# Optimization experiments

Hardware: AMD Instinct MI355X
Metric: run time of the kernel (lower is better)

Reference implementation:

```python
import jax, jax.numpy as jnp
import numpy as np

B, S_ENC, S_DEC = 4, 2048, 1024
ENC_DIM, DEC_DIM, H = 1024, 1024, 16
CROSS_DIM = max(ENC_DIM, DEC_DIM)
HEAD_DIM_DEC = DEC_DIM // H
SCALE = HEAD_DIM_DEC ** 0.5  # module divides by dec_scaling only


def _linear_params(key, d_in, d_out):
    kw, kb = jax.random.split(key)
    bound = 1.0 / np.sqrt(d_in)
    W = jax.random.uniform(kw, (d_in, d_out), jnp.float32, -bound, bound)
    b = jax.random.uniform(kb, (d_out,), jnp.float32, -bound, bound)
    return W, b


def setup_inputs() -> dict:
    key = jax.random.key(0)
    ks = jax.random.split(key, 7)
    enc = jax.random.normal(ks[0], (B, S_ENC, ENC_DIM), jnp.float32)
    dec = jax.random.normal(ks[1], (B, S_DEC, DEC_DIM), jnp.float32)
    enc_mask = jax.random.uniform(ks[2], (B, 1, 1, S_ENC)) < 0.1
    q_w, q_b = _linear_params(ks[3], DEC_DIM, CROSS_DIM)
    k_w, k_b = _linear_params(ks[4], ENC_DIM, CROSS_DIM)
    v_w, v_b = _linear_params(ks[5], ENC_DIM, DEC_DIM)
    o_w, o_b = _linear_params(ks[6], DEC_DIM, DEC_DIM)
    return {"enc": enc, "enc_mask": enc_mask, "dec": dec,
            "q_w": q_w, "q_b": q_b, "k_w": k_w, "k_b": k_b,
            "v_w": v_w, "v_b": v_b, "o_w": o_w, "o_b": o_b}


def _split_heads(x):
    b, s, d = x.shape
    return x.reshape(b, s, H, d // H).transpose(0, 2, 1, 3)  # [b,h,s,hd]


def reference(enc, enc_mask, dec, q_w, q_b, k_w, k_b, v_w, v_b, o_w, o_b):
    q = _split_heads(dec @ q_w + q_b)   # [B,H,Sq,cross_hd]
    k = _split_heads(enc @ k_w + k_b)   # [B,H,Sk,cross_hd]
    v = _split_heads(enc @ v_w + v_b)   # [B,H,Sk,dec_hd]
    logits = jnp.einsum('bhqd,bhkd->bhqk', q, k) / SCALE
    logits = jnp.where(enc_mask, -jnp.inf, logits)
    a = jax.nn.softmax(logits, axis=-1)
    x = jnp.einsum('bhqk,bhkd->bhqd', a, v)          # [B,H,Sq,dec_hd]
    x = x.transpose(0, 2, 1, 3).reshape(x.shape[0], x.shape[2], -1)  # [B,Sq,DEC_DIM]
    return x @ o_w + o_b
```

## Files before the change

kernel.cpp:

```cpp
#include <hip/hip_runtime.h>
#include <hip/hip_bf16.h>
#include <cstdint>

#define BB   4
#define SENC 2048
#define SDEC 1024
#define DM   1024
#define NH   16
#define HD   64

using short8 = __attribute__((ext_vector_type(8))) short;
using f32x4  = __attribute__((ext_vector_type(4))) float;

__device__ inline unsigned short f2bf(float f) {
    return (unsigned short)((__builtin_bit_cast(unsigned int, f) + 0x8000u) >> 16);
}
__device__ inline unsigned int pk2bf(float a, float b) {
    return ((__builtin_bit_cast(unsigned int, a) + 0x8000u) >> 16) |
           ((__builtin_bit_cast(unsigned int, b) + 0x8000u) & 0xffff0000u);
}

__device__ inline float fexp2(float x) {
#if __has_builtin(__builtin_amdgcn_exp2f)
    return __builtin_amdgcn_exp2f(x);
#else
    return exp2f(x);
#endif
}

#if __has_builtin(__builtin_amdgcn_global_load_lds)
#define HAS_GLL 1
#endif

__device__ inline void stage16(const void* g, void* l) {
#ifdef HAS_GLL
    typedef __attribute__((address_space(1))) const unsigned int guint;
    typedef __attribute__((address_space(3))) unsigned int luint;
    __builtin_amdgcn_global_load_lds((guint*)g, (luint*)l, 16, 0, 0);
#else
    *(short8*)l = *(const short8*)g;
#endif
}

__global__ __launch_bounds__(256) void prep_kernel(
    const float* __restrict__ dec, const float* __restrict__ enc,
    unsigned short* __restrict__ actb,
    const float* __restrict__ qw, const float* __restrict__ kw,
    const float* __restrict__ vw, const float* __restrict__ ow,
    unsigned short* __restrict__ qwt, unsigned short* __restrict__ kvwt,
    unsigned short* __restrict__ owt) {
    __shared__ float t[64][65];
    const int id = blockIdx.x, tid = threadIdx.x;
    if (id < 12288) {
        const int nd = BB * SDEC * DM;
        int i = (id * 256 + tid) * 4;
        const float* src = (i < nd) ? (dec + i) : (enc + (i - nd));
        float4 v = *(const float4*)src;
        ushort4 o;
        o.x = f2bf(v.x); o.y = f2bf(v.y); o.z = f2bf(v.z); o.w = f2bf(v.w);
        *(ushort4*)(actb + i) = o;
        return;
    }
    const int id2 = id - 12288;
    const int z = id2 >> 8, ky = (id2 >> 4) & 15, nx = id2 & 15;
    const float* src; unsigned short* dst;
    switch (z) {
        case 0:  src = qw; dst = qwt; break;
        case 1:  src = kw; dst = kvwt; break;
        case 2:  src = vw; dst = kvwt + (size_t)64 * 16384; break;
        default: src = ow; dst = owt; break;
    }
    const int k0 = ky * 64, n0 = nx * 64;
    #pragma unroll
    for (int it = 0; it < 16; ++it) {
        int e = it * 256 + tid, r = e >> 6, c = e & 63;
        t[r][c] = src[(size_t)(k0 + r) * DM + n0 + c];
    }
    __syncthreads();
    #pragma unroll
    for (int it = 0; it < 16; ++it) {
        int e = it * 256 + tid, r = e >> 6, c = e & 63;
        size_t off = (size_t)((n0 + r) >> 4) * 16384 + (size_t)((k0 + c) >> 3) * 128
                   + ((r & 15) << 3) + (c & 7);
        dst[off] = f2bf(t[c][r]);
    }
}

__global__ __launch_bounds__(256) void gemm_qkv_kernel(
    const unsigned short* __restrict__ encb, const unsigned short* __restrict__ decb,
    const unsigned short* __restrict__ kvwt, const unsigned short* __restrict__ qwt,
    const float* __restrict__ q_b, const float* __restrict__ k_b, const float* __restrict__ v_b,
    unsigned short* __restrict__ Qb, unsigned short* __restrict__ Kb,
    unsigned short* __restrict__ Vtb) {
    __shared__ __align__(16) unsigned short As[2][128 * 32];
    const int id = blockIdx.x;
    const bool isKV = id < 1024;
    const unsigned short *A, *Bw;
    int m0, n0;
    if (isKV) {
        const int x = id & 7, w = id >> 3;
        A = encb; Bw = kvwt;
        m0 = (x * 8 + (w >> 4)) * 128;
        n0 = (w & 15) * 128;
    } else {
        const int i2 = id - 1024, x = i2 & 7, w = i2 >> 3;
        A = decb; Bw = qwt;
        m0 = (x * 4 + (w >> 3)) * 128;
        n0 = (w & 7) * 128;
    }
    const int tid = threadIdx.x;
    const int wave = tid >> 6, lane = tid & 63, quad = lane >> 4, l16 = lane & 15;
    const int wr = wave >> 1, wc = wave & 1;
    const int r16 = lane >> 2, c8 = (lane & 3) * 8;
    f32x4 acc[4][4] = {};

    const unsigned short* Bbase = Bw + (size_t)(n0 >> 4) * 16384 + (size_t)(wc * 4) * 16384
                                + quad * 128 + l16 * 8;
    short8 bcur[4], bnxt[4];
    #pragma unroll
    for (int j = 0; j < 4; ++j) bcur[j] = *(const short8*)&Bbase[j * 16384];

    #pragma unroll
    for (int i = 0; i < 2; ++i) {
        const int row = wave * 32 + i * 16 + r16;
        stage16(&A[(size_t)(m0 + row) * DM + c8], &As[0][row * 32 + c8]);
    }
    for (int it = 0; it < 32; ++it) {
        const int bf = it & 1;
        __syncthreads();
        if (it < 31) {
            const int kb2 = (it + 1) * 32, nb = bf ^ 1;
            #pragma unroll
            for (int i = 0; i < 2; ++i) {
                const int row = wave * 32 + i * 16 + r16;
                stage16(&A[(size_t)(m0 + row) * DM + kb2 + c8], &As[nb][row * 32 + c8]);
            }
            #pragma unroll
            for (int j = 0; j < 4; ++j)
                bnxt[j] = *(const short8*)&Bbase[j * 16384 + kb2 * 16];
        }
        short8 af[4];
        #pragma unroll
        for (int i = 0; i < 4; ++i) af[i] = *(const short8*)&As[bf][(wr * 64 + i * 16 + l16) * 32 + quad * 8];
        #pragma unroll
        for (int i = 0; i < 4; ++i)
            #pragma unroll
            for (int j = 0; j < 4; ++j)
                acc[i][j] = __builtin_amdgcn_mfma_f32_16x16x32_bf16(af[i], bcur[j], acc[i][j], 0, 0, 0);
        #pragma unroll
        for (int j = 0; j < 4; ++j) bcur[j] = bnxt[j];
    }
    #pragma unroll
    for (int i = 0; i < 4; ++i) {
        #pragma unroll
        for (int j = 0; j < 4; ++j) {
            const int gc = n0 + wc * 64 + j * 16 + l16;
            const int gr0 = m0 + wr * 64 + i * 16 + quad * 4;
            if (!isKV) {
                const float bv = q_b[gc];
                const int h = gc >> 6, d = gc & 63;
                #pragma unroll
                for (int rr = 0; rr < 4; ++rr) {
                    int gr = gr0 + rr, b = gr >> 10, sq = gr & 1023;
                    float v = (acc[i][j][rr] + bv) * 0.18033688011112042f;
                    Qb[(((size_t)(b * NH + h) * SDEC + sq) << 6) + d] = f2bf(v);
                }
            } else if (gc < 1024) {
                const float bv = k_b[gc];
                const int h = gc >> 6, d = gc & 63;
                #pragma unroll
                for (int rr = 0; rr < 4; ++rr) {
                    int gr = gr0 + rr, b = gr >> 11, sk = gr & 2047;
                    size_t off = (size_t)(b * NH + h) * 131072 + (size_t)(sk >> 4) * 1024
                               + ((d >> 3) << 7) + ((sk & 15) << 3) + (d & 7);
                    Kb[off] = f2bf(acc[i][j][rr] + bv);
                }
            } else {
                const int gc2 = gc & 1023;
                const float bv = v_b[gc2];
                const int h = gc2 >> 6, d = gc2 & 63;
                const int b = gr0 >> 11, sk0 = gr0 & 2047;
                size_t off = (size_t)(b * NH + h) * 131072 + (size_t)(d >> 4) * 32768
                           + (size_t)(sk0 >> 3) * 128 + ((d & 15) << 3) + (sk0 & 7);
                uint2 pk;
                pk.x = pk2bf(acc[i][j][0] + bv, acc[i][j][1] + bv);
                pk.y = pk2bf(acc[i][j][2] + bv, acc[i][j][3] + bv);
                *(uint2*)&Vtb[off] = pk;
            }
        }
    }
}

__global__ __launch_bounds__(256) void gemm_o_kernel(const unsigned short* __restrict__ A,
                                                     const unsigned short* __restrict__ Bw,
                                                     const float* __restrict__ bias,
                                                     float* __restrict__ Cout) {
    __shared__ __align__(16) unsigned short As[2][64 * 32];
    const int id = blockIdx.x, x = id & 7, w = id >> 3;
    const int m0 = (x * 8 + (w >> 3)) * 64, n0 = (w & 7) * 128;
    const int tid = threadIdx.x;
    const int wave = tid >> 6, lane = tid & 63, quad = lane >> 4, l16 = lane & 15;
    const int r16 = lane >> 2, c8 = (lane & 3) * 8;
    f32x4 acc[4][2] = {};
    const unsigned short* Bbase = Bw + (size_t)((n0 >> 4) + wave * 2) * 16384 + quad * 128 + l16 * 8;
    short8 bcur[2], bnxt[2];
    #pragma unroll
    for (int j = 0; j < 2; ++j) bcur[j] = *(const short8*)&Bbase[j * 16384];
    {
        const int rowA = wave * 16 + r16;
        stage16(&A[(size_t)(m0 + rowA) * DM + c8], &As[0][rowA * 32 + c8]);
    }
    for (int it = 0; it < 32; ++it) {
        const int bf = it & 1;
        __syncthreads();
        if (it < 31) {
            const int kb2 = (it + 1) * 32, nb = bf ^ 1;
            const int rowA = wave * 16 + r16;
            stage16(&A[(size_t)(m0 + rowA) * DM + kb2 + c8], &As[nb][rowA * 32 + c8]);
            #pragma unroll
            for (int j = 0; j < 2; ++j) bnxt[j] = *(const short8*)&Bbase[j * 16384 + kb2 * 16];
        }
        short8 af[4];
        #pragma unroll
        for (int i = 0; i < 4; ++i) af[i] = *(const short8*)&As[bf][(i * 16 + l16) * 32 + quad * 8];
        #pragma unroll
        for (int i = 0; i < 4; ++i)
            #pragma unroll
            for (int j = 0; j < 2; ++j)
                acc[i][j] = __builtin_amdgcn_mfma_f32_16x16x32_bf16(af[i], bcur[j], acc[i][j], 0, 0, 0);
        #pragma unroll
        for (int j = 0; j < 2; ++j) bcur[j] = bnxt[j];
    }
    #pragma unroll
    for (int i = 0; i < 4; ++i)
        #pragma unroll
        for (int j = 0; j < 2; ++j) {
            const int gc = n0 + wave * 32 + j * 16 + l16;
            const float bv = bias[gc];
            #pragma unroll
            for (int rr = 0; rr < 4; ++rr) {
                const int gr = m0 + i * 16 + quad * 4 + rr;
                Cout[(size_t)gr * DM + gc] = acc[i][j][rr] + bv;
            }
        }
}

__global__ __launch_bounds__(256) void attn_kernel(const unsigned short* __restrict__ Qb,
                                                   const unsigned short* __restrict__ Kb,
                                                   const unsigned short* __restrict__ Vtb,
                                                   const int* __restrict__ mask,
                                                   unsigned short* __restrict__ Xb) {
    __shared__ __align__(16) unsigned short Ps[4][16 * 72];
    const int id = blockIdx.x, x = id & 7, r = id >> 3;
    const int bh = x * 8 + (r & 7), qt = r >> 3;
    const int b = bh >> 4, h = bh & 15;
    const int q0 = qt * 128;
    const int tid = threadIdx.x, wave = tid >> 6, lane = tid & 63;
    const int quad = lane >> 4, l16 = lane & 15;
    const int lo = quad * 128 + l16 * 8;

    const unsigned short* Kfp = Kb + (size_t)bh * 131072;
    const unsigned short* Vfp = Vtb + (size_t)bh * 131072;
    const int* mp = mask + (size_t)b * SENC;

    short8 qf[2][2];
    {
        const unsigned short* Qp = Qb + ((size_t)bh * SDEC + q0 + wave * 32) * HD;
        #pragma unroll
        for (int g = 0; g < 2; ++g) {
            qf[g][0] = *(const short8*)&Qp[(g * 16 + l16) * HD + quad * 8];
            qf[g][1] = *(const short8*)&Qp[(g * 16 + l16) * HD + 32 + quad * 8];
        }
    }

    float lsum[2] = {0.f, 0.f};
    f32x4 o[2][4] = {};

    for (int kb = 0; kb < SENC; kb += 64) {
        short8 kA0[4], kA1[4], vB0[4], vB1[4];
        const unsigned short* kt = Kfp + (size_t)(kb >> 4) * 1024 + lo;
        const unsigned short* vt = Vfp + (size_t)(kb >> 3) * 128 + lo;
        #pragma unroll
        for (int j = 0; j < 4; ++j) {
            kA0[j] = *(const short8*)&kt[j * 1024];
            kA1[j] = *(const short8*)&kt[j * 1024 + 512];
            vB0[j] = *(const short8*)&vt[j * 32768];
            vB1[j] = *(const short8*)&vt[j * 32768 + 512];
        }
        int4 mi[4];
        #pragma unroll
        for (int j = 0; j < 4; ++j) mi[j] = *(const int4*)&mp[kb + j * 16 + quad * 4];
        #pragma unroll
        for (int g = 0; g < 2; ++g) {
            f32x4 st[4];
            #pragma unroll
            for (int j = 0; j < 4; ++j) {
                f32x4 z = {0.f, 0.f, 0.f, 0.f};
                z = __builtin_amdgcn_mfma_f32_16x16x32_bf16(kA0[j], qf[g][0], z, 0, 0, 0);
                st[j] = __builtin_amdgcn_mfma_f32_16x16x32_bf16(kA1[j], qf[g][1], z, 0, 0, 0);
            }
            #pragma unroll
            for (int j = 0; j < 4; ++j) {
                float p0 = mi[j].x ? 0.f : fexp2(st[j][0]);
                float p1 = mi[j].y ? 0.f : fexp2(st[j][1]);
                float p2 = mi[j].z ? 0.f : fexp2(st[j][2]);
                float p3 = mi[j].w ? 0.f : fexp2(st[j][3]);
                lsum[g] += (p0 + p1) + (p2 + p3);
                uint2 pkv;
                pkv.x = pk2bf(p0, p1);
                pkv.y = pk2bf(p2, p3);
                *(uint2*)&Ps[wave][l16 * 72 + j * 16 + quad * 4] = pkv;
            }
            asm volatile("s_waitcnt lgkmcnt(0)" ::: "memory");
            short8 pA0 = *(const short8*)&Ps[wave][l16 * 72 + quad * 8];
            short8 pA1 = *(const short8*)&Ps[wave][l16 * 72 + 32 + quad * 8];
            #pragma unroll
            for (int dj = 0; dj < 4; ++dj) {
                o[g][dj] = __builtin_amdgcn_mfma_f32_16x16x32_bf16(pA0, vB0[dj], o[g][dj], 0, 0, 0);
                o[g][dj] = __builtin_amdgcn_mfma_f32_16x16x32_bf16(pA1, vB1[dj], o[g][dj], 0, 0, 0);
            }
        }
    }
    #pragma unroll
    for (int g = 0; g < 2; ++g) {
        float lg = lsum[g];
        lg += __shfl_xor(lg, 16);
        lg += __shfl_xor(lg, 32);
        #pragma unroll
        for (int rr = 0; rr < 4; ++rr) {
            float iv = 1.0f / __shfl(lg, quad * 4 + rr, 64);
            int sq = q0 + wave * 32 + g * 16 + quad * 4 + rr;
            #pragma unroll
            for (int dj = 0; dj < 4; ++dj)
                Xb[((size_t)(b * SDEC) + sq) * DM + h * HD + dj * 16 + l16] = f2bf(o[g][dj][rr] * iv);
        }
    }
}

extern "C" void kernel_launch(void* const* d_in, const int* in_sizes, int n_in,
                              void* d_out, int out_size, void* d_ws, size_t ws_size,
                              hipStream_t stream) {
    const float* enc   = (const float*)d_in[0];
    const int*   emask = (const int*)d_in[1];
    const float* dec   = (const float*)d_in[2];
    const float* q_w   = (const float*)d_in[3];
    const float* q_b   = (const float*)d_in[4];
    const float* k_w   = (const float*)d_in[5];
    const float* k_b   = (const float*)d_in[6];
    const float* v_w   = (const float*)d_in[7];
    const float* v_b   = (const float*)d_in[8];
    const float* o_w   = (const float*)d_in[9];
    const float* o_b   = (const float*)d_in[10];
    float* out = (float*)d_out;

    char* ws = (char*)d_ws;
    unsigned short* decb = (unsigned short*)ws; ws += (size_t)4096 * 1024 * 2;
    unsigned short* encb = (unsigned short*)ws; ws += (size_t)8192 * 1024 * 2;
    unsigned short* qwt  = (unsigned short*)ws; ws += (size_t)1024 * 1024 * 2;
    unsigned short* kvwt = (unsigned short*)ws; ws += (size_t)2048 * 1024 * 2;
    unsigned short* owt  = (unsigned short*)ws; ws += (size_t)1024 * 1024 * 2;
    unsigned short* Qb   = (unsigned short*)ws; ws += (size_t)BB * NH * SDEC * HD * 2;
    unsigned short* Kb   = (unsigned short*)ws; ws += (size_t)BB * NH * SENC * HD * 2;
    unsigned short* Vtb  = (unsigned short*)ws; ws += (size_t)BB * NH * HD * SENC * 2;
    unsigned short* Xb   = (unsigned short*)ws; ws += (size_t)4096 * 1024 * 2;

    prep_kernel<<<13312, 256, 0, stream>>>(dec, enc, decb, q_w, k_w, v_w, o_w, qwt, kvwt, owt);
    gemm_qkv_kernel<<<1280, 256, 0, stream>>>(encb, decb, kvwt, qwt, q_b, k_b, v_b, Qb, Kb, Vtb);
    attn_kernel<<<512, 256, 0, stream>>>(Qb, Kb, Vtb, emask, Xb);
    gemm_o_kernel<<<512, 256, 0, stream>>>(Xb, owt, o_b, out);
}
```

Measured before the change: 253.9 us.

## Pre-swizzle activations into MFMA fragment layout and drop LDS staging in GEMMs

The prep kernel now writes dec/enc bf16 activations in the 16x8 fragment-tiled layout, and attention writes X in the same layout. Both GEMMs can then load A fragments directly from global memory into registers with register double-buffering, removing LDS staging and the per-iteration block barriers. Attention halves the query tile per block, which doubles the grid, and software-prefetches K. The mask is converted to an additive float bias, so the per-element select becomes an add before exp2. The costs are a transpose-like write pattern in prep and more global and L2 traffic, because A fragments are no longer shared through LDS across waves.

```diff
diff --git a/kernel.cpp b/kernel.cpp
--- a/kernel.cpp
+++ b/kernel.cpp
@@ -28,40 +28,50 @@
 #endif
 }
 
-#if __has_builtin(__builtin_amdgcn_global_load_lds)
-#define HAS_GLL 1
-#endif
-
-__device__ inline void stage16(const void* g, void* l) {
-#ifdef HAS_GLL
-    typedef __attribute__((address_space(1))) const unsigned int guint;
-    typedef __attribute__((address_space(3))) unsigned int luint;
-    __builtin_amdgcn_global_load_lds((guint*)g, (luint*)l, 16, 0, 0);
-#else
-    *(short8*)l = *(const short8*)g;
-#endif
+__device__ inline size_t frag_off(int m, int k) {
+    return (size_t)(m >> 4) * 16384 + (size_t)(k >> 3) * 128 + ((m & 15) << 3) + (k & 7);
 }
 
 __global__ __launch_bounds__(256) void prep_kernel(
     const float* __restrict__ dec, const float* __restrict__ enc,
-    unsigned short* __restrict__ actb,
+    unsigned short* __restrict__ decb, unsigned short* __restrict__ encb,
     const float* __restrict__ qw, const float* __restrict__ kw,
     const float* __restrict__ vw, const float* __restrict__ ow,
     unsigned short* __restrict__ qwt, unsigned short* __restrict__ kvwt,
-    unsigned short* __restrict__ owt) {
+    unsigned short* __restrict__ owt,
+    const int* __restrict__ mask, float* __restrict__ maskf) {
+    const int id = blockIdx.x, tid = threadIdx.x;
+    if (id < 3072) {
+        __shared__ unsigned short t[64][72];
+        const int rt = id >> 4, ct = id & 15, k0 = ct * 64;
+        const float* src; unsigned short* dst; int m0;
+        if (rt < 64) { src = dec; dst = decb; m0 = rt * 64; }
+        else         { src = enc; dst = encb; m0 = (rt - 64) * 64; }
+        #pragma unroll
+        for (int i = 0; i < 4; ++i) {
+            const int row = i * 16 + (tid >> 4), col4 = (tid & 15) * 4;
+            float4 v = *(const float4*)&src[(size_t)(m0 + row) * DM + k0 + col4];
+            ushort4 o;
+            o.x = f2bf(v.x); o.y = f2bf(v.y); o.z = f2bf(v.z); o.w = f2bf(v.w);
+            *(ushort4*)&t[row][col4] = o;
+        }
+        __syncthreads();
+        const int f = tid >> 3, sub = tid & 7;
+        const int mt = f >> 3, kc = f & 7;
+        const int row0 = mt * 16 + sub * 2;
+        short8 a = *(const short8*)&t[row0][kc * 8];
+        short8 b = *(const short8*)&t[row0 + 1][kc * 8];
+        size_t off = (size_t)(m0 / 16 + mt) * 16384 + (size_t)(k0 / 8 + kc) * 128 + sub * 16;
+        *(short8*)&dst[off] = a;
+        *(short8*)&dst[off + 8] = b;
+        return;
+    }
+    if (id == 4096) {
+        for (int j = tid; j < BB * SENC; j += 256) maskf[j] = mask[j] ? -1e30f : 0.0f;
+        return;
+    }
     __shared__ float t[64][65];
-    const int id = blockIdx.x, tid = threadIdx.x;
-    if (id < 12288) {
-        const int nd = BB * SDEC * DM;
-        int i = (id * 256 + tid) * 4;
-        const float* src = (i < nd) ? (dec + i) : (enc + (i - nd));
-        float4 v = *(const float4*)src;
-        ushort4 o;
-        o.x = f2bf(v.x); o.y = f2bf(v.y); o.z = f2bf(v.z); o.w = f2bf(v.w);
-        *(ushort4*)(actb + i) = o;
-        return;
-    }
-    const int id2 = id - 12288;
+    const int id2 = id - 3072;
     const int z = id2 >> 8, ky = (id2 >> 4) & 15, nx = id2 & 15;
     const float* src; unsigned short* dst;
     switch (z) {
@@ -92,7 +102,6 @@
     const float* __restrict__ q_b, const float* __restrict__ k_b, const float* __restrict__ v_b,
     unsigned short* __restrict__ Qb, unsigned short* __restrict__ Kb,
     unsigned short* __restrict__ Vtb) {
-    __shared__ __align__(16) unsigned short As[2][128 * 32];
     const int id = blockIdx.x;
     const bool isKV = id < 1024;
     const unsigned short *A, *Bw;
@@ -111,44 +120,33 @@
     const int tid = threadIdx.x;
     const int wave = tid >> 6, lane = tid & 63, quad = lane >> 4, l16 = lane & 15;
     const int wr = wave >> 1, wc = wave & 1;
-    const int r16 = lane >> 2, c8 = (lane & 3) * 8;
+    const int lo = quad * 128 + l16 * 8;
+    const unsigned short* Ap = A + (size_t)(m0 / 16 + wr * 4) * 16384 + lo;
+    const unsigned short* Bp = Bw + (size_t)(n0 / 16 + wc * 4) * 16384 + lo;
     f32x4 acc[4][4] = {};
-
-    const unsigned short* Bbase = Bw + (size_t)(n0 >> 4) * 16384 + (size_t)(wc * 4) * 16384
-                                + quad * 128 + l16 * 8;
-    short8 bcur[4], bnxt[4];
-    #pragma unroll
-    for (int j = 0; j < 4; ++j) bcur[j] = *(const short8*)&Bbase[j * 16384];
-
-    #pragma unroll
-    for (int i = 0; i < 2; ++i) {
-        const int row = wave * 32 + i * 16 + r16;
-        stage16(&A[(size_t)(m0 + row) * DM + c8], &As[0][row * 32 + c8]);
-    }
+    short8 ac[4], bc[4], an[4], bn[4];
+    #pragma unroll
+    for (int i = 0; i < 4; ++i) {
+        ac[i] = *(const short8*)&Ap[i * 16384];
+        bc[i] = *(const short8*)&Bp[i * 16384];
+    }
+    #pragma unroll 2
     for (int it = 0; it < 32; ++it) {
-        const int bf = it & 1;
-        __syncthreads();
         if (it < 31) {
-            const int kb2 = (it + 1) * 32, nb = bf ^ 1;
-            #pragma unroll
-            for (int i = 0; i < 2; ++i) {
-                const int row = wave * 32 + i * 16 + r16;
-                stage16(&A[(size_t)(m0 + row) * DM + kb2 + c8], &As[nb][row * 32 + c8]);
+            const int ko = (it + 1) * 512;
+            #pragma unroll
+            for (int i = 0; i < 4; ++i) {
+                an[i] = *(const short8*)&Ap[i * 16384 + ko];
+                bn[i] = *(const short8*)&Bp[i * 16384 + ko];
             }
+        }
+        #pragma unroll
+        for (int i = 0; i < 4; ++i)
             #pragma unroll
             for (int j = 0; j < 4; ++j)
-                bnxt[j] = *(const short8*)&Bbase[j * 16384 + kb2 * 16];
-        }
-        short8 af[4];
-        #pragma unroll
-        for (int i = 0; i < 4; ++i) af[i] = *(const short8*)&As[bf][(wr * 64 + i * 16 + l16) * 32 + quad * 8];
-        #pragma unroll
-        for (int i = 0; i < 4; ++i)
-            #pragma unroll
-            for (int j = 0; j < 4; ++j)
-                acc[i][j] = __builtin_amdgcn_mfma_f32_16x16x32_bf16(af[i], bcur[j], acc[i][j], 0, 0, 0);
-        #pragma unroll
-        for (int j = 0; j < 4; ++j) bcur[j] = bnxt[j];
+                acc[i][j] = __builtin_amdgcn_mfma_f32_16x16x32_bf16(ac[i], bc[j], acc[i][j], 0, 0, 0);
+        #pragma unroll
+        for (int i = 0; i < 4; ++i) { ac[i] = an[i]; bc[i] = bn[i]; }
     }
     #pragma unroll
     for (int i = 0; i < 4; ++i) {
@@ -195,41 +193,37 @@
                                                      const unsigned short* __restrict__ Bw,
                                                      const float* __restrict__ bias,
                                                      float* __restrict__ Cout) {
-    __shared__ __align__(16) unsigned short As[2][64 * 32];
     const int id = blockIdx.x, x = id & 7, w = id >> 3;
     const int m0 = (x * 8 + (w >> 3)) * 64, n0 = (w & 7) * 128;
     const int tid = threadIdx.x;
     const int wave = tid >> 6, lane = tid & 63, quad = lane >> 4, l16 = lane & 15;
-    const int r16 = lane >> 2, c8 = (lane & 3) * 8;
+    const int lo = quad * 128 + l16 * 8;
+    const unsigned short* Ap = A + (size_t)(m0 / 16) * 16384 + lo;
+    const unsigned short* Bp = Bw + (size_t)(n0 / 16 + wave * 2) * 16384 + lo;
     f32x4 acc[4][2] = {};
-    const unsigned short* Bbase = Bw + (size_t)((n0 >> 4) + wave * 2) * 16384 + quad * 128 + l16 * 8;
-    short8 bcur[2], bnxt[2];
-    #pragma unroll
-    for (int j = 0; j < 2; ++j) bcur[j] = *(const short8*)&Bbase[j * 16384];
-    {
-        const int rowA = wave * 16 + r16;
-        stage16(&A[(size_t)(m0 + rowA) * DM + c8], &As[0][rowA * 32 + c8]);
-    }
+    short8 ac[4], bc[2], an[4], bn[2];
+    #pragma unroll
+    for (int i = 0; i < 4; ++i) ac[i] = *(const short8*)&Ap[i * 16384];
+    #pragma unroll
+    for (int j = 0; j < 2; ++j) bc[j] = *(const short8*)&Bp[j * 16384];
+    #pragma unroll 2
     for (int it = 0; it < 32; ++it) {
-        const int bf = it & 1;
-        __syncthreads();
         if (it < 31) {
-            const int kb2 = (it + 1) * 32, nb = bf ^ 1;
-            const int rowA = wave * 16 + r16;
-            stage16(&A[(size_t)(m0 + rowA) * DM + kb2 + c8], &As[nb][rowA * 32 + c8]);
-            #pragma unroll
-            for (int j = 0; j < 2; ++j) bnxt[j] = *(const short8*)&Bbase[j * 16384 + kb2 * 16];
-        }
-        short8 af[4];
-        #pragma unroll
-        for (int i = 0; i < 4; ++i) af[i] = *(const short8*)&As[bf][(i * 16 + l16) * 32 + quad * 8];
+            const int ko = (it + 1) * 512;
+            #pragma unroll
+            for (int i = 0; i < 4; ++i) an[i] = *(const short8*)&Ap[i * 16384 + ko];
+            #pragma unroll
+            for (int j = 0; j < 2; ++j) bn[j] = *(const short8*)&Bp[j * 16384 + ko];
+        }
         #pragma unroll
         for (int i = 0; i < 4; ++i)
             #pragma unroll
             for (int j = 0; j < 2; ++j)
-                acc[i][j] = __builtin_amdgcn_mfma_f32_16x16x32_bf16(af[i], bcur[j], acc[i][j], 0, 0, 0);
-        #pragma unroll
-        for (int j = 0; j < 2; ++j) bcur[j] = bnxt[j];
+                acc[i][j] = __builtin_amdgcn_mfma_f32_16x16x32_bf16(ac[i], bc[j], acc[i][j], 0, 0, 0);
+        #pragma unroll
+        for (int i = 0; i < 4; ++i) ac[i] = an[i];
+        #pragma unroll
+        for (int j = 0; j < 2; ++j) bc[j] = bn[j];
     }
     #pragma unroll
     for (int i = 0; i < 4; ++i)
@@ -248,91 +242,101 @@
 __global__ __launch_bounds__(256) void attn_kernel(const unsigned short* __restrict__ Qb,
                                                    const unsigned short* __restrict__ Kb,
                                                    const unsigned short* __restrict__ Vtb,
-                                                   const int* __restrict__ mask,
+                                                   const float* __restrict__ maskf,
                                                    unsigned short* __restrict__ Xb) {
     __shared__ __align__(16) unsigned short Ps[4][16 * 72];
     const int id = blockIdx.x, x = id & 7, r = id >> 3;
     const int bh = x * 8 + (r & 7), qt = r >> 3;
     const int b = bh >> 4, h = bh & 15;
-    const int q0 = qt * 128;
+    const int q0 = qt * 64;
     const int tid = threadIdx.x, wave = tid >> 6, lane = tid & 63;
     const int quad = lane >> 4, l16 = lane & 15;
     const int lo = quad * 128 + l16 * 8;
 
-    const unsigned short* Kfp = Kb + (size_t)bh * 131072;
-    const unsigned short* Vfp = Vtb + (size_t)bh * 131072;
-    const int* mp = mask + (size_t)b * SENC;
-
-    short8 qf[2][2];
+    const unsigned short* Kfp = Kb + (size_t)bh * 131072 + lo;
+    const unsigned short* Vfp = Vtb + (size_t)bh * 131072 + lo;
+    const float* mp = maskf + (size_t)b * SENC;
+
+    short8 qf0, qf1;
     {
-        const unsigned short* Qp = Qb + ((size_t)bh * SDEC + q0 + wave * 32) * HD;
-        #pragma unroll
-        for (int g = 0; g < 2; ++g) {
-            qf[g][0] = *(const short8*)&Qp[(g * 16 + l16) * HD + quad * 8];
-            qf[g][1] = *(const short8*)&Qp[(g * 16 + l16) * HD + 32 + quad * 8];
-        }
-    }
-
-    float lsum[2] = {0.f, 0.f};
-    f32x4 o[2][4] = {};
-
-    for (int kb = 0; kb < SENC; kb += 64) {
-        short8 kA0[4], kA1[4], vB0[4], vB1[4];
-        const unsigned short* kt = Kfp + (size_t)(kb >> 4) * 1024 + lo;
-        const unsigned short* vt = Vfp + (size_t)(kb >> 3) * 128 + lo;
+        const unsigned short* Qp = Qb + ((size_t)bh * SDEC + q0 + wave * 16) * HD;
+        qf0 = *(const short8*)&Qp[l16 * HD + quad * 8];
+        qf1 = *(const short8*)&Qp[l16 * HD + 32 + quad * 8];
+    }
+
+    float lsum = 0.f;
+    f32x4 o[4] = {};
+    short8 kc0[4], kc1[4], kn0[4], kn1[4];
+    #pragma unroll
+    for (int j = 0; j < 4; ++j) {
+        kc0[j] = *(const short8*)&Kfp[j * 1024];
+        kc1[j] = *(const short8*)&Kfp[j * 1024 + 512];
+    }
+
+    #pragma unroll 2
+    for (int it = 0; it < SENC / 64; ++it) {
+        const int kb = it * 64;
+        short8 vB0[4], vB1[4];
+        const unsigned short* vt = Vfp + (size_t)(kb >> 3) * 128;
         #pragma unroll
         for (int j = 0; j < 4; ++j) {
-            kA0[j] = *(const short8*)&kt[j * 1024];
-            kA1[j] = *(const short8*)&kt[j * 1024 + 512];
             vB0[j] = *(const short8*)&vt[j * 32768];
             vB1[j] = *(const short8*)&vt[j * 32768 + 512];
         }
-        int4 mi[4];
-        #pragma unroll
-        for (int j = 0; j < 4; ++j) mi[j] = *(const int4*)&mp[kb + j * 16 + quad * 4];
-        #pragma unroll
-        for (int g = 0; g < 2; ++g) {
-            f32x4 st[4];
+        float4 mf[4];
+        #pragma unroll
+        for (int j = 0; j < 4; ++j) mf[j] = *(const float4*)&mp[kb + j * 16 + quad * 4];
+        f32x4 st[4];
+        #pragma unroll
+        for (int j = 0; j < 4; ++j) {
+            f32x4 z = {0.f, 0.f, 0.f, 0.f};
+            z = __builtin_amdgcn_mfma_f32_16x16x32_bf16(kc0[j], qf0, z, 0, 0, 0);
+            st[j] = __builtin_amdgcn_mfma_f32_16x16x32_bf16(kc1[j], qf1, z, 0, 0, 0);
+        }
+        if (it + 1 < SENC / 64) {
+            const unsigned short* kt = Kfp + (size_t)((it + 1) * 4) * 1024;
             #pragma unroll
             for (int j = 0; j < 4; ++j) {
-                f32x4 z = {0.f, 0.f, 0.f, 0.f};
-                z = __builtin_amdgcn_mfma_f32_16x16x32_bf16(kA0[j], qf[g][0], z, 0, 0, 0);
-                st[j] = __builtin_amdgcn_mfma_f32_16x16x32_bf16(kA1[j], qf[g][1], z, 0, 0, 0);
+                kn0[j] = *(const short8*)&kt[j * 1024];
+                kn1[j] = *(const short8*)&kt[j * 1024 + 512];
             }
-            #pragma unroll
-            for (int j = 0; j < 4; ++j) {
-                float p0 = mi[j].x ? 0.f : fexp2(st[j][0]);
-                float p1 = mi[j].y ? 0.f : fexp2(st[j][1]);
-                float p2 = mi[j].z ? 0.f : fexp2(st[j][2]);
-                float p3 = mi[j].w ? 0.f : fexp2(st[j][3]);
-                lsum[g] += (p0 + p1) + (p2 + p3);
-                uint2 pkv;
-                pkv.x = pk2bf(p0, p1);
-                pkv.y = pk2bf(p2, p3);
-                *(uint2*)&Ps[wave][l16 * 72 + j * 16 + quad * 4] = pkv;
-            }
-            asm volatile("s_waitcnt lgkmcnt(0)" ::: "memory");
-            short8 pA0 = *(const short8*)&Ps[wave][l16 * 72 + quad * 8];
-            short8 pA1 = *(const short8*)&Ps[wave][l16 * 72 + 32 + quad * 8];
-            #pragma unroll
-            for (int dj = 0; dj < 4; ++dj) {
-                o[g][dj] = __builtin_amdgcn_mfma_f32_16x16x32_bf16(pA0, vB0[dj], o[g][dj], 0, 0, 0);
-                o[g][dj] = __builtin_amdgcn_mfma_f32_16x16x32_bf16(pA1, vB1[dj], o[g][dj], 0, 0, 0);
-            }
-        }
-    }
-    #pragma unroll
-    for (int g = 0; g < 2; ++g) {
-        float lg = lsum[g];
-        lg += __shfl_xor(lg, 16);
-        lg += __shfl_xor(lg, 32);
-        #pragma unroll
-        for (int rr = 0; rr < 4; ++rr) {
-            float iv = 1.0f / __shfl(lg, quad * 4 + rr, 64);
-            int sq = q0 + wave * 32 + g * 16 + quad * 4 + rr;
-            #pragma unroll
-            for (int dj = 0; dj < 4; ++dj)
-                Xb[((size_t)(b * SDEC) + sq) * DM + h * HD + dj * 16 + l16] = f2bf(o[g][dj][rr] * iv);
+        }
+        #pragma unroll
+        for (int j = 0; j < 4; ++j) {
+            float p0 = fexp2(st[j][0] + mf[j].x);
+            float p1 = fexp2(st[j][1] + mf[j].y);
+            float p2 = fexp2(st[j][2] + mf[j].z);
+            float p3 = fexp2(st[j][3] + mf[j].w);
+            lsum += (p0 + p1) + (p2 + p3);
+            uint2 pkv;
+            pkv.x = pk2bf(p0, p1);
+            pkv.y = pk2bf(p2, p3);
+            *(uint2*)&Ps[wave][l16 * 72 + j * 16 + quad * 4] = pkv;
+        }
+        asm volatile("s_waitcnt lgkmcnt(0)" ::: "memory");
+        short8 pA0 = *(const short8*)&Ps[wave][l16 * 72 + quad * 8];
+        short8 pA1 = *(const short8*)&Ps[wave][l16 * 72 + 32 + quad * 8];
+        #pragma unroll
+        for (int dj = 0; dj < 4; ++dj) {
+            o[dj] = __builtin_amdgcn_mfma_f32_16x16x32_bf16(pA0, vB0[dj], o[dj], 0, 0, 0);
+            o[dj] = __builtin_amdgcn_mfma_f32_16x16x32_bf16(pA1, vB1[dj], o[dj], 0, 0, 0);
+        }
+        #pragma unroll
+        for (int j = 0; j < 4; ++j) { kc0[j] = kn0[j]; kc1[j] = kn1[j]; }
+    }
+    lsum += __shfl_xor(lsum, 16);
+    lsum += __shfl_xor(lsum, 32);
+    const int mtile = b * 64 + qt * 4 + wave;
+    const int kbase = h * 64;
+    #pragma unroll
+    for (int rr = 0; rr < 4; ++rr) {
+        float iv = 1.0f / __shfl(lsum, quad * 4 + rr, 64);
+        #pragma unroll
+        for (int dj = 0; dj < 4; ++dj) {
+            const int k = kbase + dj * 16 + l16;
+            size_t off = (size_t)mtile * 16384 + (size_t)(k >> 3) * 128
+                       + ((quad * 4 + rr) << 3) + (k & 7);
+            Xb[off] = f2bf(o[dj][rr] * iv);
         }
     }
 }
@@ -363,9 +367,11 @@
     unsigned short* Kb   = (unsigned short*)ws; ws += (size_t)BB * NH * SENC * HD * 2;
     unsigned short* Vtb  = (unsigned short*)ws; ws += (size_t)BB * NH * HD * SENC * 2;
     unsigned short* Xb   = (unsigned short*)ws; ws += (size_t)4096 * 1024 * 2;
-
-    prep_kernel<<<13312, 256, 0, stream>>>(dec, enc, decb, q_w, k_w, v_w, o_w, qwt, kvwt, owt);
+    float*          mkf  = (float*)ws;          ws += (size_t)BB * SENC * 4;
+
+    prep_kernel<<<4097, 256, 0, stream>>>(dec, enc, decb, encb, q_w, k_w, v_w, o_w,
+                                          qwt, kvwt, owt, emask, mkf);
     gemm_qkv_kernel<<<1280, 256, 0, stream>>>(encb, decb, kvwt, qwt, q_b, k_b, v_b, Qb, Kb, Vtb);
-    attn_kernel<<<512, 256, 0, stream>>>(Qb, Kb, Vtb, emask, Xb);
+    attn_kernel<<<1024, 256, 0, stream>>>(Qb, Kb, Vtb, mkf, Xb);
     gemm_o_kernel<<<512, 256, 0, stream>>>(Xb, owt, o_b, out);
 }
```

Result: slower. 272.3 us (+7.3%).
